# Kernel optimization log

Measured on AMD Instinct MI355X. Metric: run time of the kernel, lower is better.

The kernel has to match this reference:

```python
import jax, jax.numpy as jnp
import numpy as np

WINDOW = 16
STRIDE = 8
PADDING = 0
EPS = 1e-6


def setup_inputs() -> dict:
    key = jax.random.key(0)
    x = jax.random.normal(key, (4, 32, 256, 256), dtype=jnp.float32)
    return {"x": x}


def reference(x):
    # Faithful translation of ExtractTensorPatches.forward:
    # grouped conv2d with an (identity + eps) one-hot kernel per channel,
    # so out_i = patch_elem_i + eps * sum(patch).
    B, C, H, W = x.shape
    w2 = WINDOW * WINDOW
    # (w2, 1, w, w): diag = 1+eps, off-diag = eps (matches create_kernel)
    k = (jnp.eye(w2, dtype=x.dtype) + jnp.asarray(EPS, x.dtype)).reshape(
        w2, 1, WINDOW, WINDOW
    )
    k = jnp.tile(k, (C, 1, 1, 1))  # (C*w2, 1, w, w), group-major like torch repeat
    out = jax.lax.conv_general_dilated(
        x,
        k,
        window_strides=(STRIDE, STRIDE),
        padding=[(PADDING, PADDING), (PADDING, PADDING)],
        feature_group_count=C,
        dimension_numbers=("NCHW", "OIHW", "NCHW"),
    )  # (B, C*w2, Ho, Wo)
    Ho, Wo = out.shape[2], out.shape[3]
    out = out.reshape(B, C, WINDOW, WINDOW, Ho * Wo)
    return jnp.transpose(out, (0, 4, 1, 2, 3))  # (B, L, C, w, w)
```

## Files before the change

kernel.cpp:

```cpp
#include <hip/hip_runtime.h>


#define BB   4
#define CC   32
#define HH   256
#define WW   256
#define STR  8
#define HOC  31
#define WOC  31
#define LL   (HOC * WOC)
#define EPSF 1e-6f
#define PITCH 272

__global__ __launch_bounds__(256) void
extract_patches_strip(const float* __restrict__ x, float* __restrict__ out) {
    __shared__ float strip[16 * PITCH];
    __shared__ float cs[16 * 32];
    __shared__ float epsP[32];

    const int tid = threadIdx.x;
    const int c   = blockIdx.x;
    const int ho  = blockIdx.y;
    const int b   = blockIdx.z;

    const float* src = x + ((size_t)(b * CC + c) * HH + (size_t)(ho * STR)) * WW;

#pragma unroll
    for (int it = 0; it < 4; ++it) {
        const int g   = (it * 256 + tid) * 4;
        const float4 v = *(const float4*)(src + g);
        const int row = g >> 8;
        const int col = g & 255;
        *(float4*)(&strip[row * PITCH + col]) = v;
        float s4 = v.x + v.y + v.z + v.w;
        s4 += __shfl_xor(s4, 1, 64);
        if ((tid & 1) == 0)
            cs[g >> 3] = s4;
    }
    __syncthreads();

    if (tid < WOC) {
        float s = 0.f;
#pragma unroll
        for (int r = 0; r < 16; ++r)
            s += cs[r * 32 + 2 * tid] + cs[r * 32 + 2 * tid + 1];
        epsP[tid] = EPSF * s;
    }
    __syncthreads();

    const int wave  = tid >> 6;
    const int lane  = tid & 63;
    const int prow  = lane >> 2;
    const int pcol4 = (lane & 3) * 4;
    float* dstbase = out
        + (((size_t)b * LL + (size_t)ho * WOC) * CC + c) * 256
        + (size_t)(lane * 4);
#pragma unroll
    for (int p = 0; p < 8; ++p) {
        const int wo = p * 4 + wave;
        if (wo < WOC) {
            const float4 v =
                *(const float4*)(&strip[prow * PITCH + wo * STR + pcol4]);
            const float e = epsP[wo];
            const float4 o = make_float4(v.x + e, v.y + e, v.z + e, v.w + e);
            *(float4*)(dstbase + ((size_t)wo << 13)) = o;
        }
    }
}

extern "C" void kernel_launch(void* const* d_in, const int* in_sizes, int n_in,
                              void* d_out, int out_size, void* d_ws, size_t ws_size,
                              hipStream_t stream) {
    const float* x = (const float*)d_in[0];
    float* out = (float*)d_out;

    dim3 grid(CC, HOC, BB);
    dim3 block(256);
    extract_patches_strip<<<grid, block, 0, stream>>>(x, out);
}
```

Before: 148.6 us.

## Roll 8-row groups through a 3-slot shared ring to reuse overlapping patch rows

Each block now handles up to four consecutive output rows and keeps 8-row input groups in a rotating three-slot shared-memory ring. Each overlapping group is loaded and column-summed once instead of twice, which removes the duplicated input reads. Output writes switch to nontemporal stores. The grid shrinks from 31 to 8 row segments, so there is less parallelism and more barriers per block.

```diff
diff --git a/kernel.cpp b/kernel.cpp
--- a/kernel.cpp
+++ b/kernel.cpp
@@ -11,60 +11,87 @@
 #define LL   (HOC * WOC)
 #define EPSF 1e-6f
 #define PITCH 272
+#define SLOT  (8 * PITCH)
+
+typedef float v4f __attribute__((ext_vector_type(4)));
 
 __global__ __launch_bounds__(256) void
-extract_patches_strip(const float* __restrict__ x, float* __restrict__ out) {
-    __shared__ float strip[16 * PITCH];
-    __shared__ float cs[16 * 32];
-    __shared__ float epsP[32];
+extract_patches_roll(const float* __restrict__ x, float* __restrict__ out) {
+    __shared__ float strip[3 * SLOT];
+    __shared__ float cs[3 * 256];
+    __shared__ float gs[3 * 32];
 
     const int tid = threadIdx.x;
     const int c   = blockIdx.x;
-    const int ho  = blockIdx.y;
+    const int seg = blockIdx.y;
     const int b   = blockIdx.z;
 
-    const float* src = x + ((size_t)(b * CC + c) * HH + (size_t)(ho * STR)) * WW;
+    const int ho0 = seg * 4;
+    const int nho = (seg == 7) ? 3 : 4;
 
+    const float* xb = x + ((size_t)(b * CC + c) * HH) * WW;
+
+    auto load_group = [&](int G, int slot) {
 #pragma unroll
-    for (int it = 0; it < 4; ++it) {
-        const int g   = (it * 256 + tid) * 4;
-        const float4 v = *(const float4*)(src + g);
-        const int row = g >> 8;
-        const int col = g & 255;
-        *(float4*)(&strip[row * PITCH + col]) = v;
-        float s4 = v.x + v.y + v.z + v.w;
-        s4 += __shfl_xor(s4, 1, 64);
-        if ((tid & 1) == 0)
-            cs[g >> 3] = s4;
-    }
+        for (int it = 0; it < 2; ++it) {
+            const int idx = it * 256 + tid;
+            const int g   = idx * 4;
+            const v4f v = *(const v4f*)(xb + (size_t)G * 2048 + g);
+            const int row = g >> 8;
+            const int col = g & 255;
+            *(v4f*)(&strip[slot * SLOT + row * PITCH + col]) = v;
+            float s4 = v.x + v.y + v.z + v.w;
+            s4 += __shfl_xor(s4, 1, 64);
+            if ((tid & 1) == 0) cs[slot * 256 + (idx >> 1)] = s4;
+        }
+    };
+    auto gsum = [&](int slot) {
+        if (tid < WOC) {
+            float s = 0.f;
+#pragma unroll
+            for (int r = 0; r < 8; ++r)
+                s += cs[slot * 256 + r * 32 + 2 * tid]
+                   + cs[slot * 256 + r * 32 + 2 * tid + 1];
+            gs[slot * 32 + tid] = s;
+        }
+    };
+
+    load_group(ho0 + 0, 0);
+    load_group(ho0 + 1, 1);
     __syncthreads();
+    gsum(0);
+    gsum(1);
 
-    if (tid < WOC) {
-        float s = 0.f;
-#pragma unroll
-        for (int r = 0; r < 16; ++r)
-            s += cs[r * 32 + 2 * tid] + cs[r * 32 + 2 * tid + 1];
-        epsP[tid] = EPSF * s;
-    }
-    __syncthreads();
-
+    const int lane  = tid & 63;
     const int wave  = tid >> 6;
-    const int lane  = tid & 63;
     const int prow  = lane >> 2;
     const int pcol4 = (lane & 3) * 4;
-    float* dstbase = out
-        + (((size_t)b * LL + (size_t)ho * WOC) * CC + c) * 256
-        + (size_t)(lane * 4);
+
+    for (int j = 0; j < nho; ++j) {
+        const int sj  = j % 3;
+        const int sj1 = (j + 1) % 3;
+        const int sj2 = (j + 2) % 3;
+        if (j + 2 <= nho) load_group(ho0 + j + 2, sj2);
+        __syncthreads();
+        if (j + 2 <= nho) gsum(sj2);
+
+        const int ho = ho0 + j;
+        float* dst0 = out + (((size_t)(b * LL + ho * WOC) * CC + c) << 8)
+                    + (size_t)(lane * 4);
 #pragma unroll
-    for (int p = 0; p < 8; ++p) {
-        const int wo = p * 4 + wave;
-        if (wo < WOC) {
-            const float4 v =
-                *(const float4*)(&strip[prow * PITCH + wo * STR + pcol4]);
-            const float e = epsP[wo];
-            const float4 o = make_float4(v.x + e, v.y + e, v.z + e, v.w + e);
-            *(float4*)(dstbase + ((size_t)wo << 13)) = o;
+        for (int p = 0; p < 8; ++p) {
+            const int wo = p * 4 + wave;
+            if (wo < WOC) {
+                const int slot = (prow < 8) ? sj : sj1;
+                const v4f v = *(const v4f*)(
+                    &strip[slot * SLOT + (prow & 7) * PITCH + wo * STR + pcol4]);
+                const float e = EPSF * (gs[sj * 32 + wo] + gs[sj1 * 32 + wo]);
+                v4f o;
+                o.x = v.x + e; o.y = v.y + e; o.z = v.z + e; o.w = v.w + e;
+                __builtin_nontemporal_store(o, (v4f*)(dst0 + ((size_t)wo << 13)));
+            }
         }
+        __syncthreads();
     }
 }
 
@@ -74,7 +101,7 @@
     const float* x = (const float*)d_in[0];
     float* out = (float*)d_out;
 
-    dim3 grid(CC, HOC, BB);
+    dim3 grid(CC, 8, BB);
     dim3 block(256);
-    extract_patches_strip<<<grid, block, 0, stream>>>(x, out);
+    extract_patches_roll<<<grid, block, 0, stream>>>(x, out);
 }
```

Result: no change. 150.3 us (+1.2%).
